# Optimization experiments

Hardware: AMD Instinct MI355X
Metric: run time of the kernel (lower is better)

## Reference

```python
import jax, jax.numpy as jnp
import numpy as np

VOCAB = 100000
EMBED = 128
N_INNER = VOCAB - 1
MAX_PATH = 20
BATCH = 32768


def setup_inputs() -> dict:
    key = jax.random.key(0)
    k1, k2, k3, k4, k5, k6, k7 = jax.random.split(key, 7)
    center = jax.random.randint(k1, (BATCH,), 0, VOCAB)
    target = jax.random.randint(k2, (BATCH,), 0, VOCAB)
    # embedding table (module inits uniform(-0.5/d, 0.5/d)); inner vectors init zero,
    # but we use small random values so gradients/scores are non-trivial.
    init_range = 0.5 / EMBED
    in_emb = jax.random.uniform(k3, (VOCAB, EMBED), jnp.float32, -init_range, init_range)
    inner_vec = jax.random.normal(k4, (N_INNER, EMBED), jnp.float32) * 0.01
    # Huffman buffers: per-word path lengths between 8 and MAX_PATH, padded with 0.
    lengths = jax.random.randint(k5, (VOCAB, 1), 8, MAX_PATH + 1)          # (V,1)
    pos = jnp.arange(MAX_PATH)[None, :]                                     # (1,L)
    masks = (pos < lengths).astype(jnp.float32)                             # (V,L)
    paths = jax.random.randint(k6, (VOCAB, MAX_PATH), 0, N_INNER) * (pos < lengths)
    # codes are +/-1 on valid positions (word2vec sign labels), 0 on padding
    codes = (2.0 * jax.random.randint(k7, (VOCAB, MAX_PATH), 0, 2).astype(jnp.float32) - 1.0) * masks
    return {"center": center, "target": target, "in_emb": in_emb,
            "inner_vec": inner_vec, "paths": paths, "codes": codes, "masks": masks}


def reference(center, target, in_emb, inner_vec, paths, codes, masks):
    h = in_emb[center]                      # (B, D) center word vectors
    p = paths[target]                       # (B, L) inner-node ids along Huffman path
    c = codes[target]                       # (B, L) +/-1 direction labels
    m = masks[target]                       # (B, L) valid-position mask
    iv = inner_vec[p]                       # (B, L, D) gathered inner-node vectors
    scores = jnp.einsum('bld,bd->bl', iv, h)            # batched matvec
    log_probs = jax.nn.log_sigmoid(c * scores)          # (B, L)
    loss = -(log_probs * m).sum(axis=1)                 # masked path sum
    return loss.mean()
```

## Files before the change

kernel.cpp:

```cpp
#include <hip/hip_runtime.h>

#define VOCAB 100000
#define EMBED 128
#define MAX_PATH 20
#define BATCH 32768
#define WPB 4
#define NBLOCKS (BATCH / WPB)

__global__ __launch_bounds__(256, 4) void hs_loss_kernel(
    const int* __restrict__ center, const int* __restrict__ target,
    const float* __restrict__ in_emb, const float* __restrict__ inner_vec,
    const int* __restrict__ paths, const float* __restrict__ codes,
    float* __restrict__ partials)
{
    __shared__ float4 lds_buf[WPB * 640];

    const int wave = threadIdx.x >> 6;
    const int lane = threadIdx.x & 63;
    const int g    = lane >> 4;
    const int gl   = lane & 15;
    const int b = blockIdx.x * WPB + wave;

    const int c = center[b];
    const int t = target[b];

    const float4* hp = (const float4*)(in_emb + (size_t)c * EMBED);
    const float4 h0 = hp[gl];
    const float4 h1 = hp[gl + 16];

    const int base = t * MAX_PATH + g;
    int   p[5];
    float cd[5];
    #pragma unroll
    for (int j = 0; j < 5; ++j) {
        p[j]  = paths[base + 4 * j];
        cd[j] = codes[base + 4 * j];
    }

    float4* myl = lds_buf + wave * 640;
    #pragma unroll
    for (int j = 0; j < 5; ++j) {
        const float* src = inner_vec + (size_t)p[j] * EMBED + 4 * gl;
        __builtin_amdgcn_global_load_lds(
            (const __attribute__((address_space(1))) unsigned int*)(src),
            (__attribute__((address_space(3))) unsigned int*)(myl + j * 128),
            16, 0, 0);
        __builtin_amdgcn_global_load_lds(
            (const __attribute__((address_space(1))) unsigned int*)(src + 64),
            (__attribute__((address_space(3))) unsigned int*)(myl + j * 128 + 64),
            16, 0, 0);
    }
    __syncthreads();

    float acc = 0.f;
    #pragma unroll
    for (int j = 0; j < 5; ++j) {
        const float4 a0 = myl[j * 128 + lane];
        const float4 a1 = myl[j * 128 + 64 + lane];
        float d = h0.x * a0.x;
        d = fmaf(h0.y, a0.y, d);
        d = fmaf(h0.z, a0.z, d);
        d = fmaf(h0.w, a0.w, d);
        float e = h1.x * a1.x;
        e = fmaf(h1.y, a1.y, e);
        e = fmaf(h1.z, a1.z, e);
        e = fmaf(h1.w, a1.w, e);
        d += e;
        d += __shfl_xor(d, 1, 64);
        d += __shfl_xor(d, 2, 64);
        d += __shfl_xor(d, 4, 64);
        d += __shfl_xor(d, 8, 64);
        const float x  = cd[j] * d;
        const float ls = fminf(x, 0.f) - __logf(1.f + __expf(-fabsf(x)));
        acc = fmaf(fabsf(cd[j]), ls, acc);
    }

    acc += __shfl_xor(acc, 16, 64);
    acc += __shfl_xor(acc, 32, 64);

    __shared__ float ws[WPB];
    if (lane == 0) ws[wave] = -acc;
    __syncthreads();
    if (threadIdx.x == 0) {
        partials[blockIdx.x] = ws[0] + ws[1] + ws[2] + ws[3];
    }
}

__global__ __launch_bounds__(256) void hs_reduce_kernel(
    const float* __restrict__ partials, float* __restrict__ out)
{
    const float4* p4 = (const float4*)partials;
    float s = 0.f;
    #pragma unroll
    for (int i = 0; i < NBLOCKS / 4 / 256; ++i) {
        const float4 v = p4[i * 256 + threadIdx.x];
        s += (v.x + v.y) + (v.z + v.w);
    }
    #pragma unroll
    for (int off = 32; off; off >>= 1) s += __shfl_xor(s, off, 64);
    __shared__ float ws[4];
    const int wave = threadIdx.x >> 6;
    const int lane = threadIdx.x & 63;
    if (lane == 0) ws[wave] = s;
    __syncthreads();
    if (threadIdx.x == 0) {
        out[0] = (ws[0] + ws[1] + ws[2] + ws[3]) / (float)BATCH;
    }
}

extern "C" void kernel_launch(void* const* d_in, const int* in_sizes, int n_in,
                              void* d_out, int out_size, void* d_ws, size_t ws_size,
                              hipStream_t stream) {
    const int*   center    = (const int*)d_in[0];
    const int*   target    = (const int*)d_in[1];
    const float* in_emb    = (const float*)d_in[2];
    const float* inner_vec = (const float*)d_in[3];
    const int*   paths     = (const int*)d_in[4];
    const float* codes     = (const float*)d_in[5];
    float* out = (float*)d_out;
    float* partials = (float*)d_ws;

    hs_loss_kernel<<<NBLOCKS, 256, 0, stream>>>(
        center, target, in_emb, inner_vec, paths, codes, partials);
    hs_reduce_kernel<<<1, 256, 0, stream>>>(partials, out);
}
```

Measured before the change: 168.7 us.

## Split each sample's path into 5 blocks and drop LDS staging

Each block now handles one chunk of four path nodes per sample, so five times as many blocks are launched and each thread loads its inner vector straight into registers instead of staging it through LDS with async global-to-LDS copies. The aim is more parallelism and memory-level concurrency with less LDS use and a lighter per-block footprint. In exchange the center embedding, target index loads and block reduction are repeated five times, the partials array grows fivefold, and each thread has fewer loads in flight.

```diff
diff --git a/kernel.cpp b/kernel.cpp
--- a/kernel.cpp
+++ b/kernel.cpp
@@ -5,21 +5,23 @@
 #define MAX_PATH 20
 #define BATCH 32768
 #define WPB 4
-#define NBLOCKS (BATCH / WPB)
+#define NCHUNK 5
+#define NBLK (BATCH / WPB * NCHUNK)
 
-__global__ __launch_bounds__(256, 4) void hs_loss_kernel(
+__global__ __launch_bounds__(256) void hs_loss_kernel(
     const int* __restrict__ center, const int* __restrict__ target,
     const float* __restrict__ in_emb, const float* __restrict__ inner_vec,
     const int* __restrict__ paths, const float* __restrict__ codes,
     float* __restrict__ partials)
 {
-    __shared__ float4 lds_buf[WPB * 640];
-
+    const int bid  = blockIdx.x;
+    const int x    = bid / NCHUNK;
+    const int k    = bid - NCHUNK * x;
     const int wave = threadIdx.x >> 6;
     const int lane = threadIdx.x & 63;
     const int g    = lane >> 4;
     const int gl   = lane & 15;
-    const int b = blockIdx.x * WPB + wave;
+    const int b    = x * WPB + wave;
 
     const int c = center[b];
     const int t = target[b];
@@ -27,53 +29,31 @@
     const float4* hp = (const float4*)(in_emb + (size_t)c * EMBED);
     const float4 h0 = hp[gl];
     const float4 h1 = hp[gl + 16];
+    const int   node = k * 4 + g;
+    const int   idx  = t * MAX_PATH + node;
+    const int   p    = paths[idx];
+    const float cd   = codes[idx];
 
-    const int base = t * MAX_PATH + g;
-    int   p[5];
-    float cd[5];
-    #pragma unroll
-    for (int j = 0; j < 5; ++j) {
-        p[j]  = paths[base + 4 * j];
-        cd[j] = codes[base + 4 * j];
-    }
+    const float4* ivp = (const float4*)(inner_vec + (size_t)p * EMBED);
+    const float4 a0 = ivp[gl];
+    const float4 a1 = ivp[gl + 16];
 
-    float4* myl = lds_buf + wave * 640;
-    #pragma unroll
-    for (int j = 0; j < 5; ++j) {
-        const float* src = inner_vec + (size_t)p[j] * EMBED + 4 * gl;
-        __builtin_amdgcn_global_load_lds(
-            (const __attribute__((address_space(1))) unsigned int*)(src),
-            (__attribute__((address_space(3))) unsigned int*)(myl + j * 128),
-            16, 0, 0);
-        __builtin_amdgcn_global_load_lds(
-            (const __attribute__((address_space(1))) unsigned int*)(src + 64),
-            (__attribute__((address_space(3))) unsigned int*)(myl + j * 128 + 64),
-            16, 0, 0);
-    }
-    __syncthreads();
-
-    float acc = 0.f;
-    #pragma unroll
-    for (int j = 0; j < 5; ++j) {
-        const float4 a0 = myl[j * 128 + lane];
-        const float4 a1 = myl[j * 128 + 64 + lane];
-        float d = h0.x * a0.x;
-        d = fmaf(h0.y, a0.y, d);
-        d = fmaf(h0.z, a0.z, d);
-        d = fmaf(h0.w, a0.w, d);
-        float e = h1.x * a1.x;
-        e = fmaf(h1.y, a1.y, e);
-        e = fmaf(h1.z, a1.z, e);
-        e = fmaf(h1.w, a1.w, e);
-        d += e;
-        d += __shfl_xor(d, 1, 64);
-        d += __shfl_xor(d, 2, 64);
-        d += __shfl_xor(d, 4, 64);
-        d += __shfl_xor(d, 8, 64);
-        const float x  = cd[j] * d;
-        const float ls = fminf(x, 0.f) - __logf(1.f + __expf(-fabsf(x)));
-        acc = fmaf(fabsf(cd[j]), ls, acc);
-    }
+    float d = h0.x * a0.x;
+    d = fmaf(h0.y, a0.y, d);
+    d = fmaf(h0.z, a0.z, d);
+    d = fmaf(h0.w, a0.w, d);
+    float e = h1.x * a1.x;
+    e = fmaf(h1.y, a1.y, e);
+    e = fmaf(h1.z, a1.z, e);
+    e = fmaf(h1.w, a1.w, e);
+    d += e;
+    d += __shfl_xor(d, 1, 64);
+    d += __shfl_xor(d, 2, 64);
+    d += __shfl_xor(d, 4, 64);
+    d += __shfl_xor(d, 8, 64);
+    const float xx = cd * d;
+    const float ls = fminf(xx, 0.f) - __logf(1.f + __expf(-fabsf(xx)));
+    float acc = fabsf(cd) * ls;
 
     acc += __shfl_xor(acc, 16, 64);
     acc += __shfl_xor(acc, 32, 64);
@@ -82,7 +62,7 @@
     if (lane == 0) ws[wave] = -acc;
     __syncthreads();
     if (threadIdx.x == 0) {
-        partials[blockIdx.x] = ws[0] + ws[1] + ws[2] + ws[3];
+        partials[bid] = ws[0] + ws[1] + ws[2] + ws[3];
     }
 }
 
@@ -92,7 +72,7 @@
     const float4* p4 = (const float4*)partials;
     float s = 0.f;
     #pragma unroll
-    for (int i = 0; i < NBLOCKS / 4 / 256; ++i) {
+    for (int i = 0; i < NBLK / 4 / 256; ++i) {
         const float4 v = p4[i * 256 + threadIdx.x];
         s += (v.x + v.y) + (v.z + v.w);
     }
@@ -120,7 +100,7 @@
     float* out = (float*)d_out;
     float* partials = (float*)d_ws;
 
-    hs_loss_kernel<<<NBLOCKS, 256, 0, stream>>>(
+    hs_loss_kernel<<<NBLK, 256, 0, stream>>>(
         center, target, in_emb, inner_vec, paths, codes, partials);
     hs_reduce_kernel<<<1, 256, 0, stream>>>(partials, out);
 }
```

New measurement: 183.4 us. +8.7%, slower.

## Split inner-vector gathers between registers and LDS, skip padded path rows

Applied to the files above, without the earlier changes.

The first two path rows per lane group are now loaded straight into registers, and only the remaining three go through LDS via global_load_lds. Rows 3 and 4 are skipped when every code in the wave is zero, i.e. padding, which saves gather bandwidth. The LDS buffer shrinks and launch bounds rise to 6 blocks per CU to allow more occupancy. The block-wide __syncthreads is replaced by a per-wave waitcnt plus sched_barrier, which relies on the hand-encoded waitcnt value being correct for LDS-DMA completion.

```diff
diff --git a/kernel.cpp b/kernel.cpp
--- a/kernel.cpp
+++ b/kernel.cpp
@@ -7,13 +7,14 @@
 #define WPB 4
 #define NBLOCKS (BATCH / WPB)
 
-__global__ __launch_bounds__(256, 4) void hs_loss_kernel(
+__global__ __launch_bounds__(256, 6) void hs_loss_kernel(
     const int* __restrict__ center, const int* __restrict__ target,
     const float* __restrict__ in_emb, const float* __restrict__ inner_vec,
     const int* __restrict__ paths, const float* __restrict__ codes,
     float* __restrict__ partials)
 {
-    __shared__ float4 lds_buf[WPB * 640];
+    __shared__ float4 lds_buf[WPB * 384];
+    __shared__ float  ws[WPB];
 
     const int wave = threadIdx.x >> 6;
     const int lane = threadIdx.x & 63;
@@ -36,27 +37,81 @@
         p[j]  = paths[base + 4 * j];
         cd[j] = codes[base + 4 * j];
     }
+    const bool do3 = __ballot(cd[3] != 0.f) != 0ull;
+    const bool do4 = __ballot(cd[4] != 0.f) != 0ull;
 
-    float4* myl = lds_buf + wave * 640;
-    #pragma unroll
-    for (int j = 0; j < 5; ++j) {
-        const float* src = inner_vec + (size_t)p[j] * EMBED + 4 * gl;
+    const float4* v0 = (const float4*)(inner_vec + (size_t)p[0] * EMBED);
+    const float4 r00 = v0[gl], r01 = v0[gl + 16];
+    const float4* v1 = (const float4*)(inner_vec + (size_t)p[1] * EMBED);
+    const float4 r10 = v1[gl], r11 = v1[gl + 16];
+
+    float4* myl = lds_buf + wave * 384;
+    {
+        const float* src = inner_vec + (size_t)p[2] * EMBED + 4 * gl;
         __builtin_amdgcn_global_load_lds(
             (const __attribute__((address_space(1))) unsigned int*)(src),
-            (__attribute__((address_space(3))) unsigned int*)(myl + j * 128),
+            (__attribute__((address_space(3))) unsigned int*)(myl),
             16, 0, 0);
         __builtin_amdgcn_global_load_lds(
             (const __attribute__((address_space(1))) unsigned int*)(src + 64),
-            (__attribute__((address_space(3))) unsigned int*)(myl + j * 128 + 64),
+            (__attribute__((address_space(3))) unsigned int*)(myl + 64),
             16, 0, 0);
     }
-    __syncthreads();
+    if (do3) {
+        const float* src = inner_vec + (size_t)p[3] * EMBED + 4 * gl;
+        __builtin_amdgcn_global_load_lds(
+            (const __attribute__((address_space(1))) unsigned int*)(src),
+            (__attribute__((address_space(3))) unsigned int*)(myl + 128),
+            16, 0, 0);
+        __builtin_amdgcn_global_load_lds(
+            (const __attribute__((address_space(1))) unsigned int*)(src + 64),
+            (__attribute__((address_space(3))) unsigned int*)(myl + 192),
+            16, 0, 0);
+    }
+    if (do4) {
+        const float* src = inner_vec + (size_t)p[4] * EMBED + 4 * gl;
+        __builtin_amdgcn_global_load_lds(
+            (const __attribute__((address_space(1))) unsigned int*)(src),
+            (__attribute__((address_space(3))) unsigned int*)(myl + 256),
+            16, 0, 0);
+        __builtin_amdgcn_global_load_lds(
+            (const __attribute__((address_space(1))) unsigned int*)(src + 64),
+            (__attribute__((address_space(3))) unsigned int*)(myl + 320),
+            16, 0, 0);
+    }
 
     float acc = 0.f;
     #pragma unroll
-    for (int j = 0; j < 5; ++j) {
-        const float4 a0 = myl[j * 128 + lane];
-        const float4 a1 = myl[j * 128 + 64 + lane];
+    for (int j = 0; j < 2; ++j) {
+        const float4 a0 = (j == 0) ? r00 : r10;
+        const float4 a1 = (j == 0) ? r01 : r11;
+        float d = h0.x * a0.x;
+        d = fmaf(h0.y, a0.y, d);
+        d = fmaf(h0.z, a0.z, d);
+        d = fmaf(h0.w, a0.w, d);
+        float e = h1.x * a1.x;
+        e = fmaf(h1.y, a1.y, e);
+        e = fmaf(h1.z, a1.z, e);
+        e = fmaf(h1.w, a1.w, e);
+        d += e;
+        d += __shfl_xor(d, 1, 64);
+        d += __shfl_xor(d, 2, 64);
+        d += __shfl_xor(d, 4, 64);
+        d += __shfl_xor(d, 8, 64);
+        const float x  = cd[j] * d;
+        const float ls = fminf(x, 0.f) - __logf(1.f + __expf(-fabsf(x)));
+        acc = fmaf(fabsf(cd[j]), ls, acc);
+    }
+
+    __builtin_amdgcn_s_waitcnt(0xF70);
+    __builtin_amdgcn_sched_barrier(0);
+
+    #pragma unroll
+    for (int j = 2; j < 5; ++j) {
+        if (j == 3 && !do3) continue;
+        if (j == 4 && !do4) continue;
+        const float4 a0 = myl[(j - 2) * 128 + lane];
+        const float4 a1 = myl[(j - 2) * 128 + 64 + lane];
         float d = h0.x * a0.x;
         d = fmaf(h0.y, a0.y, d);
         d = fmaf(h0.z, a0.z, d);
@@ -78,7 +133,6 @@
     acc += __shfl_xor(acc, 16, 64);
     acc += __shfl_xor(acc, 32, 64);
 
-    __shared__ float ws[WPB];
     if (lane == 0) ws[wave] = -acc;
     __syncthreads();
     if (threadIdx.x == 0) {
```

Result: faster. 158.4 us, median of 2 (-6.1%).
